# Performance work log

Hardware: AMD Instinct MI355X
Metric: run time of the kernel (lower is better)

Reference implementation:

```python
import jax, jax.numpy as jnp
import numpy as np

N_QUBITS = 14
N_LAYERS = 4
BATCH = 2048
DIM = 2 ** N_QUBITS


def setup_inputs() -> dict:
    key = jax.random.key(0)
    k1, k2 = jax.random.split(key)
    x = jax.random.normal(k1, (BATCH, N_QUBITS), dtype=jnp.float32)
    params = 2.0 * jnp.pi * jax.random.uniform(k2, (N_LAYERS, 1, N_QUBITS), dtype=jnp.float32)
    return {"x": x, "params": params}


def _angle_embed_x(x):
    """RX(x_q) angle embedding from |0...0>: product state, qubit 0 most significant."""
    B, n = x.shape
    c = jnp.cos(x / 2)
    s = jnp.sin(x / 2)
    state = jnp.ones((B, 1), dtype=jnp.complex64)
    for q in range(n):  # fixed small loop over qubits (kron build-up)
        amp = jnp.stack([c[:, q] + 0j, (-1j) * s[:, q]], axis=-1).astype(jnp.complex64)  # (B,2)
        state = (state[:, :, None] * amp[:, None, :]).reshape(B, -1)
    return state  # (B, 2^n)


def _apply_rx(state, theta, q, n):
    """Apply RX(theta) on qubit q to batched state (B, 2^n)."""
    c = jnp.cos(theta / 2).astype(jnp.complex64)
    s = ((-1j) * jnp.sin(theta / 2)).astype(jnp.complex64)
    B = state.shape[0]
    st = state.reshape(B, 2 ** q, 2, 2 ** (n - q - 1))
    a0, a1 = st[:, :, 0, :], st[:, :, 1, :]
    new = jnp.stack([c * a0 + s * a1, s * a0 + c * a1], axis=2)
    return new.reshape(B, -1)


def _apply_cnot(state, ctrl, tgt, n):
    B = state.shape[0]
    lo, hi = min(ctrl, tgt), max(ctrl, tgt)
    st = state.reshape(B, 2 ** lo, 2, 2 ** (hi - lo - 1), 2, 2 ** (n - hi - 1))
    if ctrl < tgt:
        # control axis=2, target axis=4: flip target where control==1
        flipped = st[:, :, 1, :, ::-1, :]
        st = jnp.stack([st[:, :, 0], flipped], axis=2)
    else:
        # control axis=4, target axis=2
        flipped = st[:, :, ::-1, :, 1, :]
        st = jnp.stack([st[:, :, :, :, 0, :], flipped], axis=4)
    return st.reshape(B, -1)


def _z_signs(n):
    # sign[q, k] = +1 if bit q (MSB-first) of k is 0 else -1
    k = np.arange(2 ** n)
    bits = (k[None, :] >> np.arange(n - 1, -1, -1)[:, None]) & 1
    return jnp.asarray(1.0 - 2.0 * bits, dtype=jnp.float32)  # (n, 2^n)


def reference(x, params):
    n = N_QUBITS
    state = _angle_embed_x(x)  # (B, 2^n) complex64
    for layer in range(N_LAYERS):
        w = params[layer, 0]  # (n,)
        for q in range(n):
            state = _apply_rx(state, w[q], q, n)
        for q in range(n):  # ring of CNOTs (basic entangling layer)
            state = _apply_cnot(state, q, (q + 1) % n, n)
    probs = state.real ** 2 + state.imag ** 2  # (B, 2^n)
    return probs @ _z_signs(n).T  # (B, n) per-qubit <Z>
```

## Files before the change

kernel.cpp:

```cpp
#include <hip/hip_runtime.h>
#include <hip/hip_fp16.h>

#define NQ     14
#define NL     4
#define BATCH  2048
#define DIM    16384
#define BLK    512
#define NCH    (DIM / 4)
#define PCH    (NCH + NCH / 8)

using f2 = __attribute__((ext_vector_type(2))) float;
__device__ __forceinline__ f2 ff2(float a, float b) { f2 r; r.x = a; r.y = b; return r; }

__device__ __forceinline__ unsigned h2u(__half2 h) { return __builtin_bit_cast(unsigned, h); }
__device__ __forceinline__ __half2 u2h(unsigned u) { return __builtin_bit_cast(__half2, u); }
__device__ __forceinline__ unsigned sw16(unsigned u) { return __builtin_amdgcn_alignbit(u, u, 16); }

template <int K>
__device__ __forceinline__ void rot_k(__half2* X, __half2* Y, __half2 T, __half2 Sn) {
#pragma unroll
  for (int k = 0; k < 16; ++k) {
    if (!(k & K)) {
      const int k1 = k | K;
      const __half2 u1 = __hfma2(T, Y[k1], X[k]);
      const __half2 w1 = __hfma2(Sn, u1, Y[k1]);
      X[k]  = __hfma2(T, w1, u1);
      Y[k1] = w1;
      const __half2 u2 = __hfma2(T, Y[k], X[k1]);
      const __half2 w2 = __hfma2(Sn, u2, Y[k]);
      X[k1] = __hfma2(T, w2, u2);
      Y[k]  = w2;
    }
  }
}
__device__ __forceinline__ void rot0(__half2* X, __half2* Y, __half2 T, __half2 Sn) {
#pragma unroll
  for (int k = 0; k < 16; ++k) {
    const __half2 sy = __lowhigh2highlow(Y[k]);
    const __half2 u = __hfma2(T, sy, X[k]);
    const __half2 w = __hfma2(Sn, u, sy);
    X[k] = __hfma2(T, w, u);
    Y[k] = __lowhigh2highlow(w);
  }
}

__global__ __launch_bounds__(BLK)
__attribute__((amdgpu_waves_per_eu(4, 4)))
void qsim_kernel(const float* __restrict__ x,
                 const float* __restrict__ params,
                 float* __restrict__ out) {
  __shared__ uint4 lds[PCH];
  __shared__ float exc[NQ], exs[NQ];
  __shared__ uint2 gTS[NL * NQ];
  __shared__ float red[8][16];
  char* const sb = (char*)lds;

  const int b = blockIdx.x;
  const int t = threadIdx.x;

  if (t < NQ) { const float xv = x[b * NQ + t]; exc[t] = cosf(0.5f * xv); exs[t] = sinf(0.5f * xv); }
  if (t < NL * NQ) {
    float ph = 0.5f * params[t];
    if (ph > 1.5707964f) ph -= 3.14159265f;
    const float tf = tanf(0.5f * ph);
    const __half th = __float2half_rn(tf);
    const float thf = __half2float(th);
    const float sf = 2.0f * thf / (1.0f + thf * thf);
    gTS[t] = make_uint2(h2u(__half2half2(th)), h2u(__float2half2_rn(-sf)));
  }
  __syncthreads();

  __half2 X[16], Y[16];

  char* const pA = sb + 16 * (9 * t);
  char* const pB = sb + 16 * (t & 7) + 1152 * (t >> 3);
  char* const pC = sb + 16 * ((t & 63) + ((t >> 3) & 7) + 576 * (t >> 6));
  char* const pD = sb + 16 * (t + (t >> 3));

  int MA0 = 0;
  {
    const int Me[9] = {0x2007, 0x200F, 0x201F, 0x203F, 0x207F, 0x20FF, 0x21FF, 0x23FF, 0x27FF};
#pragma unroll
    for (int i = 0; i < 9; ++i) if ((t >> i) & 1) MA0 ^= Me[i];
  }
  int offD[8];
#pragma unroll
  for (int g = 0; g < 8; ++g) {
    const int Mrep = ((g & 1) ? 0x2FFF : 0) ^ ((g & 2) ? 0x3FFF : 0) ^ ((g & 4) ? 0x1FFF : 0);
    const int cT = (MA0 ^ Mrep) >> 2;
    offD[g] = 16 * (cT + (cT >> 3));
  }
  const int P = __popc(t) & 1;

  {
    float pb = 1.0f;
#pragma unroll
    for (int p = 0; p < 9; ++p) pb *= ((t >> p) & 1) ? exs[8 - p] : exc[8 - p];
    const int pct = __popc(t);
#pragma unroll
    for (int i = 0; i < 8; ++i) {
      const float fc = ((i & 1) ? exs[11] : exc[11]) * ((i & 2) ? exs[10] : exc[10]) *
                       ((i & 4) ? exs[9] : exc[9]);
      float xv[4], yv[4];
#pragma unroll
      for (int l = 0; l < 4; ++l) {
        const float fl = ((l & 1) ? exs[13] : exc[13]) * ((l & 2) ? exs[12] : exc[12]);
        const float f = pb * fc * fl;
        const int pc = (pct + __popc(i) + __popc(l)) & 3;
        xv[l] = (pc == 0) ? f : ((pc == 2) ? -f : 0.0f);
        yv[l] = (pc == 1) ? -f : ((pc == 3) ? f : 0.0f);
      }
      X[2 * i]     = __floats2half2_rn(xv[0], xv[1]);
      X[2 * i + 1] = __floats2half2_rn(xv[2], xv[3]);
      Y[2 * i]     = __floats2half2_rn(yv[0], yv[1]);
      Y[2 * i + 1] = __floats2half2_rn(yv[2], yv[3]);
    }
  }

#pragma unroll
  for (int layer = 0; layer < NL; ++layer) {
    __half2 T, Sn;
#define MKST(qi) { const uint2 g_ = gTS[layer * NQ + (qi)]; T = u2h(g_.x); Sn = u2h(g_.y); }

    if (layer > 0) {
#pragma unroll
      for (int i = 0; i < 8; ++i) {
        const uint4 u = *(const uint4*)(pA + 16 * i);
        X[2 * i] = u2h(u.x); Y[2 * i] = u2h(u.y);
        X[2 * i + 1] = u2h(u.z); Y[2 * i + 1] = u2h(u.w);
      }
    }
    MKST(13); rot0(X, Y, T, Sn);
    MKST(12); rot_k<1>(X, Y, T, Sn);
    MKST(11); rot_k<2>(X, Y, T, Sn);
    MKST(10); rot_k<4>(X, Y, T, Sn);
    MKST(9);  rot_k<8>(X, Y, T, Sn);
#pragma unroll
    for (int i = 0; i < 8; ++i)
      *(uint4*)(pA + 16 * i) = make_uint4(h2u(X[2 * i]), h2u(Y[2 * i]),
                                          h2u(X[2 * i + 1]), h2u(Y[2 * i + 1]));
    __builtin_amdgcn_wave_barrier();

#pragma unroll
    for (int m = 0; m < 8; ++m) {
      const uint4 u = *(const uint4*)(pB + 144 * m);
      X[2 * m] = u2h(u.x); Y[2 * m] = u2h(u.y);
      X[2 * m + 1] = u2h(u.z); Y[2 * m + 1] = u2h(u.w);
    }
    MKST(8); rot_k<2>(X, Y, T, Sn);
    MKST(7); rot_k<4>(X, Y, T, Sn);
    MKST(6); rot_k<8>(X, Y, T, Sn);
#pragma unroll
    for (int m = 0; m < 8; ++m)
      *(uint4*)(pB + 144 * m) = make_uint4(h2u(X[2 * m]), h2u(Y[2 * m]),
                                           h2u(X[2 * m + 1]), h2u(Y[2 * m + 1]));
    __builtin_amdgcn_wave_barrier();

#pragma unroll
    for (int m = 0; m < 8; ++m) {
      const uint4 u = *(const uint4*)(pC + 1152 * m);
      X[2 * m] = u2h(u.x); Y[2 * m] = u2h(u.y);
      X[2 * m + 1] = u2h(u.z); Y[2 * m + 1] = u2h(u.w);
    }
    MKST(5); rot_k<2>(X, Y, T, Sn);
    MKST(4); rot_k<4>(X, Y, T, Sn);
    MKST(3); rot_k<8>(X, Y, T, Sn);
#pragma unroll
    for (int m = 0; m < 8; ++m)
      *(uint4*)(pC + 1152 * m) = make_uint4(h2u(X[2 * m]), h2u(Y[2 * m]),
                                            h2u(X[2 * m + 1]), h2u(Y[2 * m + 1]));
    __syncthreads();

#pragma unroll
    for (int m = 0; m < 8; ++m) {
      const uint4 u = *(const uint4*)(pD + 9216 * m);
      X[2 * m] = u2h(u.x); Y[2 * m] = u2h(u.y);
      X[2 * m + 1] = u2h(u.z); Y[2 * m + 1] = u2h(u.w);
    }
    if (layer < NL - 1) __syncthreads();
    MKST(2); rot_k<2>(X, Y, T, Sn);
    MKST(1); rot_k<4>(X, Y, T, Sn);
    MKST(0); rot_k<8>(X, Y, T, Sn);
#undef MKST

    if (layer < NL - 1) {
#pragma unroll
      for (int g = 0; g < 8; ++g) {
        const int k0 = 2 * g;
        const unsigned w0 = __builtin_amdgcn_perm(h2u(X[k0 ^ 12]), h2u(X[k0]), 0x07060100u);
        const unsigned w1 = __builtin_amdgcn_perm(h2u(Y[k0 ^ 12]), h2u(Y[k0]), 0x07060100u);
        const unsigned w2 = __builtin_amdgcn_perm(h2u(X[k0 ^ 13]), h2u(X[k0 ^ 1]), 0x05040302u);
        const unsigned w3 = __builtin_amdgcn_perm(h2u(Y[k0 ^ 13]), h2u(Y[k0 ^ 1]), 0x05040302u);
        const bool rev = ((P ^ (__popc(g) & 1)) != 0);
        const uint4 o = make_uint4(rev ? sw16(w2) : w0, rev ? sw16(w3) : w1,
                                   rev ? sw16(w0) : w2, rev ? sw16(w1) : w3);
        *(uint4*)(sb + offD[g]) = o;
      }
      __syncthreads();
    }
  }

  {
    f2 pp[16];
#pragma unroll
    for (int k = 0; k < 16; ++k) {
      const float xl = __low2float(X[k]), xh = __high2float(X[k]);
      const float yl = __low2float(Y[k]), yh = __high2float(Y[k]);
      pp[k] = ff2(fmaf(xl, xl, yl * yl), fmaf(xh, xh, yh * yh));
    }
#pragma unroll
    for (int st = 0; st < 4; ++st) {
      const int h = 1 << st;
#pragma unroll
      for (int k = 0; k < 16; ++k) {
        if (!(k & h)) {
          const f2 u = pp[k], w = pp[k | h];
          pp[k] = u + w;
          pp[k | h] = u - w;
        }
      }
    }
    float w24 = pp[12].x + pp[12].y;
    float w28 = pp[14].x + pp[14].y;
    float w30 = pp[15].x + pp[15].y;
    float w31 = pp[15].x - pp[15].y;
    float w15 = pp[7].x - pp[7].y;

    const int lane = t & 63;
#pragma unroll
    for (int m = 0; m < 6; ++m) {
      const int h = 1 << m;
      const bool hi = (lane & h) != 0;
      float u;
      u = __shfl_xor(w28, h, 64); w28 = hi ? (u - w28) : (u + w28);
      u = __shfl_xor(w30, h, 64); w30 = hi ? (u - w30) : (u + w30);
      u = __shfl_xor(w31, h, 64); w31 = hi ? (u - w31) : (u + w31);
      u = __shfl_xor(w15, h, 64); w15 = hi ? (u - w15) : (u + w15);
      u = __shfl_xor(w24, h, 64); w24 = u + w24;
    }
    const int w = t >> 6;
    const float swv = (__popc(w) & 1) ? -1.0f : 1.0f;
    if (lane == 0) {
      red[w][1] = w24;
      red[w][2] = w28;
      red[w][3] = ((w >> 2) & 1) ? -w28 : w28;
      red[w][4] = (((w >> 1) ^ (w >> 2)) & 1) ? -w28 : w28;
      red[w][5] = swv * w28;
    } else if (lane == 32) { red[w][6]  = swv * w28; }
    else if (lane == 48)   { red[w][7]  = swv * w28; }
    else if (lane == 56)   { red[w][8]  = swv * w28; }
    else if (lane == 60)   { red[w][9]  = swv * w28; }
    else if (lane == 62)   { red[w][10] = swv * w28; }
    else if (lane == 63)   { red[w][11] = swv * w28;
                             red[w][12] = swv * w30;
                             red[w][13] = swv * w31;
                             red[w][0]  = swv * w15; }
    __syncthreads();
    if (t < NQ) {
      float sq = 0.0f;
#pragma unroll
      for (int ww = 0; ww < 8; ++ww) sq += red[ww][t];
      out[b * NQ + t] = sq;
    }
  }
}

extern "C" void kernel_launch(void* const* d_in, const int* in_sizes, int n_in,
                              void* d_out, int out_size, void* d_ws, size_t ws_size,
                              hipStream_t stream) {
  const float* x      = (const float*)d_in[0];
  const float* params = (const float*)d_in[1];
  float* out          = (float*)d_out;
  qsim_kernel<<<BATCH, BLK, 0, stream>>>(x, params, out);
}
```

Before: 183.2 us.

## Fold first-layer RX rotations into angle embedding and skip layer zero

Because RX(x) followed by RX(w) on the same qubit equals RX(x+w), the first layer's rotation angles are added to the embedding angles. The initial product state is then built directly in the layout the final-register stage of layer 0 would hold, the layer-0 CNOT scatter is applied, and the loop starts at layer 1. This removes one full layer of rotations and several LDS transpose passes with their barriers. The risk is that the re-indexed qubit-to-register mapping in the embedding must match the layer-0 output layout exactly.

```diff
diff --git a/kernel.cpp b/kernel.cpp
--- a/kernel.cpp
+++ b/kernel.cpp
@@ -44,6 +44,22 @@
   }
 }
 
+__device__ __forceinline__ void cnot_scatter(char* sb, const int* offD, int P,
+                                             const __half2* X, const __half2* Y) {
+#pragma unroll
+  for (int g = 0; g < 8; ++g) {
+    const int k0 = 2 * g;
+    const unsigned w0 = __builtin_amdgcn_perm(h2u(X[k0 ^ 12]), h2u(X[k0]), 0x07060100u);
+    const unsigned w1 = __builtin_amdgcn_perm(h2u(Y[k0 ^ 12]), h2u(Y[k0]), 0x07060100u);
+    const unsigned w2 = __builtin_amdgcn_perm(h2u(X[k0 ^ 13]), h2u(X[k0 ^ 1]), 0x05040302u);
+    const unsigned w3 = __builtin_amdgcn_perm(h2u(Y[k0 ^ 13]), h2u(Y[k0 ^ 1]), 0x05040302u);
+    const bool rev = ((P ^ (__popc(g) & 1)) != 0);
+    const uint4 o = make_uint4(rev ? sw16(w2) : w0, rev ? sw16(w3) : w1,
+                               rev ? sw16(w0) : w2, rev ? sw16(w1) : w3);
+    *(uint4*)(sb + offD[g]) = o;
+  }
+}
+
 __global__ __launch_bounds__(BLK)
 __attribute__((amdgpu_waves_per_eu(4, 4)))
 void qsim_kernel(const float* __restrict__ x,
@@ -58,8 +74,11 @@
   const int b = blockIdx.x;
   const int t = threadIdx.x;
 
-  if (t < NQ) { const float xv = x[b * NQ + t]; exc[t] = cosf(0.5f * xv); exs[t] = sinf(0.5f * xv); }
-  if (t < NL * NQ) {
+  if (t < NQ) {
+    const float xv = x[b * NQ + t] + params[t];
+    exc[t] = cosf(0.5f * xv); exs[t] = sinf(0.5f * xv);
+  }
+  if (t >= NQ && t < NL * NQ) {
     float ph = 0.5f * params[t];
     if (ph > 1.5707964f) ph -= 3.14159265f;
     const float tf = tanf(0.5f * ph);
@@ -95,40 +114,40 @@
   {
     float pb = 1.0f;
 #pragma unroll
-    for (int p = 0; p < 9; ++p) pb *= ((t >> p) & 1) ? exs[8 - p] : exc[8 - p];
+    for (int i = 0; i < 9; ++i) pb *= ((t >> i) & 1) ? exs[11 - i] : exc[11 - i];
     const int pct = __popc(t);
 #pragma unroll
-    for (int i = 0; i < 8; ++i) {
-      const float fc = ((i & 1) ? exs[11] : exc[11]) * ((i & 2) ? exs[10] : exc[10]) *
-                       ((i & 4) ? exs[9] : exc[9]);
+    for (int m = 0; m < 8; ++m) {
+      const float fm = ((m & 1) ? exs[2] : exc[2]) * ((m & 2) ? exs[1] : exc[1]) *
+                       ((m & 4) ? exs[0] : exc[0]);
       float xv[4], yv[4];
 #pragma unroll
       for (int l = 0; l < 4; ++l) {
         const float fl = ((l & 1) ? exs[13] : exc[13]) * ((l & 2) ? exs[12] : exc[12]);
-        const float f = pb * fc * fl;
-        const int pc = (pct + __popc(i) + __popc(l)) & 3;
+        const float f = pb * fm * fl;
+        const int pc = (pct + __popc(m) + __popc(l)) & 3;
         xv[l] = (pc == 0) ? f : ((pc == 2) ? -f : 0.0f);
         yv[l] = (pc == 1) ? -f : ((pc == 3) ? f : 0.0f);
       }
-      X[2 * i]     = __floats2half2_rn(xv[0], xv[1]);
-      X[2 * i + 1] = __floats2half2_rn(xv[2], xv[3]);
-      Y[2 * i]     = __floats2half2_rn(yv[0], yv[1]);
-      Y[2 * i + 1] = __floats2half2_rn(yv[2], yv[3]);
-    }
-  }
-
-#pragma unroll
-  for (int layer = 0; layer < NL; ++layer) {
+      X[2 * m]     = __floats2half2_rn(xv[0], xv[1]);
+      X[2 * m + 1] = __floats2half2_rn(xv[2], xv[3]);
+      Y[2 * m]     = __floats2half2_rn(yv[0], yv[1]);
+      Y[2 * m + 1] = __floats2half2_rn(yv[2], yv[3]);
+    }
+  }
+  cnot_scatter(sb, offD, P, X, Y);
+  __syncthreads();
+
+#pragma unroll
+  for (int layer = 1; layer < NL; ++layer) {
     __half2 T, Sn;
 #define MKST(qi) { const uint2 g_ = gTS[layer * NQ + (qi)]; T = u2h(g_.x); Sn = u2h(g_.y); }
 
-    if (layer > 0) {
-#pragma unroll
-      for (int i = 0; i < 8; ++i) {
-        const uint4 u = *(const uint4*)(pA + 16 * i);
-        X[2 * i] = u2h(u.x); Y[2 * i] = u2h(u.y);
-        X[2 * i + 1] = u2h(u.z); Y[2 * i + 1] = u2h(u.w);
-      }
+#pragma unroll
+    for (int i = 0; i < 8; ++i) {
+      const uint4 u = *(const uint4*)(pA + 16 * i);
+      X[2 * i] = u2h(u.x); Y[2 * i] = u2h(u.y);
+      X[2 * i + 1] = u2h(u.z); Y[2 * i + 1] = u2h(u.w);
     }
     MKST(13); rot0(X, Y, T, Sn);
     MKST(12); rot_k<1>(X, Y, T, Sn);
@@ -184,18 +203,7 @@
 #undef MKST
 
     if (layer < NL - 1) {
-#pragma unroll
-      for (int g = 0; g < 8; ++g) {
-        const int k0 = 2 * g;
-        const unsigned w0 = __builtin_amdgcn_perm(h2u(X[k0 ^ 12]), h2u(X[k0]), 0x07060100u);
-        const unsigned w1 = __builtin_amdgcn_perm(h2u(Y[k0 ^ 12]), h2u(Y[k0]), 0x07060100u);
-        const unsigned w2 = __builtin_amdgcn_perm(h2u(X[k0 ^ 13]), h2u(X[k0 ^ 1]), 0x05040302u);
-        const unsigned w3 = __builtin_amdgcn_perm(h2u(Y[k0 ^ 13]), h2u(Y[k0 ^ 1]), 0x05040302u);
-        const bool rev = ((P ^ (__popc(g) & 1)) != 0);
-        const uint4 o = make_uint4(rev ? sw16(w2) : w0, rev ? sw16(w3) : w1,
-                                   rev ? sw16(w0) : w2, rev ? sw16(w1) : w3);
-        *(uint4*)(sb + offD[g]) = o;
-      }
+      cnot_scatter(sb, offD, P, X, Y);
       __syncthreads();
     }
   }
```

Measured after the change: 163.0 us. -11.0%, faster.
